# Performance work log

Hardware: AMD Instinct MI355X
Metric: run time of the kernel (lower is better)

Reference implementation:

```python
import jax, jax.numpy as jnp
import numpy as np

BLOCK_LEN = 64  # chunk length l


def setup_inputs() -> dict:
    key = jax.random.key(0)
    k1, k2, k3 = jax.random.split(key, 3)
    b, s, h, p, n = 8, 4096, 16, 64, 64
    X = jax.random.normal(k1, (b, s, h, p), jnp.float32)
    # A must be negative for numerically stable decays (exp(cumsum diffs) <= 1),
    # matching real Mamba2 where A_log parameterizes a negative decay rate.
    A = -0.1 * jnp.abs(jax.random.normal(k2, (b, s, h), jnp.float32))
    B = jax.random.normal(k3, (b, s, h, n), jnp.float32)
    return {"X": X, "A": A, "B": B}


def reference(X, A, B):
    L = BLOCK_LEN
    b, s, h, p = X.shape
    n = B.shape[-1]
    c = s // L  # number of chunks

    # b (c l) ... -> b c l ...
    Xb = X.reshape(b, c, L, h, p)
    Bb = B.reshape(b, c, L, h, n)
    Ab = jnp.transpose(A.reshape(b, c, L, h), (0, 3, 1, 2))  # (b, h, c, l)

    A_cumsum = jnp.cumsum(Ab, axis=-1)  # (b, h, c, l)

    # Fused decay-einsum: states[b,c,h,p,n] =
    #   sum_l B[b,c,l,h,n] * exp(A_cumsum[b,h,c,-1] - A_cumsum[b,h,c,l]) * X[b,c,l,h,p]
    decay_states = jnp.exp(A_cumsum[..., -1:] - A_cumsum)  # (b, h, c, l)
    states = jnp.einsum('bclhn,bhcl,bclhp->bchpn', Bb, decay_states, Xb)

    # Prepend zero initial states along chunk dim -> (b, c+1, h, p, n)
    states = jnp.concatenate([jnp.zeros_like(states[:, :1]), states], axis=1)

    # Inter-chunk recurrence via exp(segsum(padded chunk totals)).
    padded_A = jnp.pad(A_cumsum[..., -1], ((0, 0), (0, 0), (1, 0)))  # (b, h, c+1)
    cs = jnp.cumsum(padded_A, axis=-1)
    Z = c + 1
    diff = cs[..., :, None] - cs[..., None, :]  # (b, h, Z, Z), row - col
    mask = jnp.tril(jnp.ones((Z, Z), dtype=bool))  # row >= col
    decay_chunk = jnp.where(mask, jnp.exp(diff), 0.0)  # (b, h, Z, Z)

    new_states = jnp.einsum('bhzc,bchpn->bzhpn', decay_chunk, states)
    return new_states[:, -1]  # (b, h, p, n)
```

## Files before the change

kernel.cpp:

```cpp
#include <hip/hip_runtime.h>
#include <hip/hip_bf16.h>


constexpr int Bn = 8;
constexpr int S  = 4096;
constexpr int H  = 16;
constexpr int P  = 64;
constexpr int N  = 64;

constexpr int NCH = 8;
constexpr int TCH = S / NCH;
constexpr int TB  = 8;

__global__ __launch_bounds__(256) void scan_weights(
    const float* __restrict__ A, float* __restrict__ W) {
  const int pair = blockIdx.x;
  const int bb = pair / H, hh = pair % H;
  const int tid = threadIdx.x;
  constexpr int TPT = S / 256;

  float vals[TPT];
  float local = 0.f;
  const int t0 = tid * TPT;
  #pragma unroll
  for (int i = 0; i < TPT; ++i) {
    float a = A[((size_t)bb * S + t0 + i) * H + hh];
    local += a;
    vals[i] = local;
  }

  __shared__ float sums[256];
  sums[tid] = local;
  __syncthreads();
  for (int off = 1; off < 256; off <<= 1) {
    float v = sums[tid];
    float add = (tid >= off) ? sums[tid - off] : 0.f;
    __syncthreads();
    sums[tid] = v + add;
    __syncthreads();
  }
  const float total = sums[255];
  const float excl  = sums[tid] - local;

  float* Wp = W + (size_t)pair * S;
  #pragma unroll
  for (int i = 0; i < TPT; ++i) {
    Wp[t0 + i] = __expf(total - (excl + vals[i]));
  }
}

__global__ __launch_bounds__(256) void outer_accum(
    const float* __restrict__ X, const float* __restrict__ Bm,
    const float* __restrict__ W, float* __restrict__ out) {
  __shared__ float Xs[TB][P];
  __shared__ float Bs[TB][N];

  const int bid  = blockIdx.x;
  const int pair = bid / NCH;
  const int ch   = bid % NCH;
  const int tid  = threadIdx.x;
  const int t_begin = ch * TCH;

  const int n0 = (tid & 15) * 4;
  const int p0 = (tid >> 4) * 4;

  const int lrow = (tid & 127) >> 4;
  const int lcol = (tid & 15) * 4;
  const bool isB = tid >= 128;

  const int bb = pair / H, hh = pair % H;
  const size_t baseX = ((size_t)bb * S * H + hh) * (size_t)P;
  const size_t baseB = ((size_t)bb * S * H + hh) * (size_t)N;
  const float* Wp = W + (size_t)pair * S;

  float acc[4][4];
  #pragma unroll
  for (int i = 0; i < 4; ++i)
    #pragma unroll
    for (int j = 0; j < 4; ++j) acc[i][j] = 0.f;

  for (int t0 = t_begin; t0 < t_begin + TCH; t0 += TB) {
    const int t = t0 + lrow;
    if (!isB) {
      const float w = Wp[t];
      const float4 v = *(const float4*)(X + baseX + (size_t)t * H * P + lcol);
      float4 sv; sv.x = v.x * w; sv.y = v.y * w; sv.z = v.z * w; sv.w = v.w * w;
      *(float4*)&Xs[lrow][lcol] = sv;
    } else {
      *(float4*)&Bs[lrow][lcol] = *(const float4*)(Bm + baseB + (size_t)t * H * N + lcol);
    }
    __syncthreads();

    #pragma unroll
    for (int tt = 0; tt < TB; ++tt) {
      const float4 xv = *(const float4*)&Xs[tt][p0];
      const float4 bv = *(const float4*)&Bs[tt][n0];
      const float xs[4] = {xv.x, xv.y, xv.z, xv.w};
      const float bs[4] = {bv.x, bv.y, bv.z, bv.w};
      #pragma unroll
      for (int i = 0; i < 4; ++i)
        #pragma unroll
        for (int j = 0; j < 4; ++j)
          acc[i][j] = fmaf(xs[i], bs[j], acc[i][j]);
    }
    __syncthreads();
  }

  float* outp = out + (size_t)pair * P * N;
  #pragma unroll
  for (int i = 0; i < 4; ++i)
    #pragma unroll
    for (int j = 0; j < 4; ++j)
      atomicAdd(&outp[(size_t)(p0 + i) * N + (n0 + j)], acc[i][j]);
}

extern "C" void kernel_launch(void* const* d_in, const int* in_sizes, int n_in,
                              void* d_out, int out_size, void* d_ws, size_t ws_size,
                              hipStream_t stream) {
  const float* X = (const float*)d_in[0];
  const float* A = (const float*)d_in[1];
  const float* B = (const float*)d_in[2];
  float* out = (float*)d_out;
  float* W   = (float*)d_ws;

  hipMemsetAsync(d_out, 0, (size_t)out_size * sizeof(float), stream);

  scan_weights<<<Bn * H, 256, 0, stream>>>(A, W);
  outer_accum<<<Bn * H * NCH, 256, 0, stream>>>(X, B, W, out);
}
```

Baseline: 327.4 us.

## Double-buffer outer-product accumulation with 8x8 register tiles and per-wave time split

```diff
diff --git a/kernel.cpp b/kernel.cpp
--- a/kernel.cpp
+++ b/kernel.cpp
@@ -1,5 +1,4 @@
 #include <hip/hip_runtime.h>
-#include <hip/hip_bf16.h>
 
 
 constexpr int Bn = 8;
@@ -10,7 +9,8 @@
 
 constexpr int NCH = 8;
 constexpr int TCH = S / NCH;
-constexpr int TB  = 8;
+constexpr int TB  = 32;
+constexpr int NIT = TCH / TB;
 
 __global__ __launch_bounds__(256) void scan_weights(
     const float* __restrict__ A, float* __restrict__ W) {
@@ -49,69 +49,138 @@
   }
 }
 
-__global__ __launch_bounds__(256) void outer_accum(
+__global__ __launch_bounds__(256, 4) void outer_accum(
     const float* __restrict__ X, const float* __restrict__ Bm,
     const float* __restrict__ W, float* __restrict__ out) {
-  __shared__ float Xs[TB][P];
-  __shared__ float Bs[TB][N];
+  __shared__ float4 lds[2][1024];
 
   const int bid  = blockIdx.x;
   const int pair = bid / NCH;
   const int ch   = bid % NCH;
   const int tid  = threadIdx.x;
+  const int lane = tid & 63;
+  const int wid  = tid >> 6;
   const int t_begin = ch * TCH;
 
-  const int n0 = (tid & 15) * 4;
-  const int p0 = (tid >> 4) * 4;
+  const int pr = (lane >> 3) * 8;
+  const int nc = (lane & 7) * 8;
 
-  const int lrow = (tid & 127) >> 4;
-  const int lcol = (tid & 15) * 4;
-  const bool isB = tid >= 128;
+  const int srow = tid >> 4;
+  const int scol = (tid & 15) * 4;
 
   const int bb = pair / H, hh = pair % H;
-  const size_t baseX = ((size_t)bb * S * H + hh) * (size_t)P;
-  const size_t baseB = ((size_t)bb * S * H + hh) * (size_t)N;
+  const float* Xp = X  + (size_t)bb * S * H * P + (size_t)hh * P + scol;
+  const float* Bp = Bm + (size_t)bb * S * H * N + (size_t)hh * N + scol;
   const float* Wp = W + (size_t)pair * S;
 
-  float acc[4][4];
+  float4 rx0, rx1, rb0, rb1;
+  float w0, w1;
+
+  auto LOAD = [&](int t0) {
+    const int ta = t0 + srow;
+    const int tb = ta + 16;
+    w0 = Wp[ta];
+    w1 = Wp[tb];
+    rx0 = *(const float4*)(Xp + (size_t)ta * (H * P));
+    rx1 = *(const float4*)(Xp + (size_t)tb * (H * P));
+    rb0 = *(const float4*)(Bp + (size_t)ta * (H * N));
+    rb1 = *(const float4*)(Bp + (size_t)tb * (H * N));
+  };
+  auto STORE = [&](int buf) {
+    float4 a = rx0; a.x *= w0; a.y *= w0; a.z *= w0; a.w *= w0;
+    float4 b = rx1; b.x *= w1; b.y *= w1; b.z *= w1; b.w *= w1;
+    lds[buf][tid]       = a;
+    lds[buf][256 + tid] = b;
+    lds[buf][512 + tid] = rb0;
+    lds[buf][768 + tid] = rb1;
+  };
+
+  float acc[8][8];
   #pragma unroll
-  for (int i = 0; i < 4; ++i)
+  for (int i = 0; i < 8; ++i)
     #pragma unroll
-    for (int j = 0; j < 4; ++j) acc[i][j] = 0.f;
+    for (int k = 0; k < 8; ++k) acc[i][k] = 0.f;
 
-  for (int t0 = t_begin; t0 < t_begin + TCH; t0 += TB) {
-    const int t = t0 + lrow;
-    if (!isB) {
-      const float w = Wp[t];
-      const float4 v = *(const float4*)(X + baseX + (size_t)t * H * P + lcol);
-      float4 sv; sv.x = v.x * w; sv.y = v.y * w; sv.z = v.z * w; sv.w = v.w * w;
-      *(float4*)&Xs[lrow][lcol] = sv;
-    } else {
-      *(float4*)&Bs[lrow][lcol] = *(const float4*)(Bm + baseB + (size_t)t * H * N + lcol);
+  LOAD(t_begin);
+  STORE(0);
+  __syncthreads();
+
+  for (int it = 0; it < NIT; ++it) {
+    const int cur = it & 1;
+    if (it + 1 < NIT) LOAD(t_begin + (it + 1) * TB);
+
+    const float* Xs = (const float*)&lds[cur][0];
+    const float* Bs = (const float*)&lds[cur][512];
+    #pragma unroll
+    for (int j = 0; j < 8; ++j) {
+      const int tt = (j << 2) | wid;
+      const float4 xa = *(const float4*)(Xs + tt * 64 + pr);
+      const float4 xb = *(const float4*)(Xs + tt * 64 + pr + 4);
+      const float4 ba = *(const float4*)(Bs + tt * 64 + nc);
+      const float4 bc = *(const float4*)(Bs + tt * 64 + nc + 4);
+      const float xs[8] = {xa.x, xa.y, xa.z, xa.w, xb.x, xb.y, xb.z, xb.w};
+      const float bs[8] = {ba.x, ba.y, ba.z, ba.w, bc.x, bc.y, bc.z, bc.w};
+      #pragma unroll
+      for (int i = 0; i < 8; ++i)
+        #pragma unroll
+        for (int k = 0; k < 8; ++k)
+          acc[i][k] = fmaf(xs[i], bs[k], acc[i][k]);
     }
-    __syncthreads();
 
-    #pragma unroll
-    for (int tt = 0; tt < TB; ++tt) {
-      const float4 xv = *(const float4*)&Xs[tt][p0];
-      const float4 bv = *(const float4*)&Bs[tt][n0];
-      const float xs[4] = {xv.x, xv.y, xv.z, xv.w};
-      const float bs[4] = {bv.x, bv.y, bv.z, bv.w};
-      #pragma unroll
-      for (int i = 0; i < 4; ++i)
-        #pragma unroll
-        for (int j = 0; j < 4; ++j)
-          acc[i][j] = fmaf(xs[i], bs[j], acc[i][j]);
+    if (it + 1 < NIT) {
+      STORE((it + 1) & 1);
+      __syncthreads();
     }
-    __syncthreads();
   }
 
-  float* outp = out + (size_t)pair * P * N;
-  #pragma unroll
-  for (int i = 0; i < 4; ++i)
+  __syncthreads();
+  float4* red = (float4*)&lds[0][0];
+
+  if (wid & 1) {
+    float4* r = red + ((wid >> 1) ? 1024 : 0) + lane;
     #pragma unroll
-    for (int j = 0; j < 4; ++j)
-      atomicAdd(&outp[(size_t)(p0 + i) * N + (n0 + j)], acc[i][j]);
+    for (int i = 0; i < 8; ++i) {
+      r[(2 * i + 0) * 64] = make_float4(acc[i][0], acc[i][1], acc[i][2], acc[i][3]);
+      r[(2 * i + 1) * 64] = make_float4(acc[i][4], acc[i][5], acc[i][6], acc[i][7]);
+    }
+  }
+  __syncthreads();
+  if (!(wid & 1)) {
+    const float4* r = red + ((wid >> 1) ? 1024 : 0) + lane;
+    #pragma unroll
+    for (int i = 0; i < 8; ++i) {
+      const float4 v0 = r[(2 * i + 0) * 64];
+      const float4 v1 = r[(2 * i + 1) * 64];
+      acc[i][0] += v0.x; acc[i][1] += v0.y; acc[i][2] += v0.z; acc[i][3] += v0.w;
+      acc[i][4] += v1.x; acc[i][5] += v1.y; acc[i][6] += v1.z; acc[i][7] += v1.w;
+    }
+  }
+  __syncthreads();
+  if (wid == 2) {
+    float4* r = red + lane;
+    #pragma unroll
+    for (int i = 0; i < 8; ++i) {
+      r[(2 * i + 0) * 64] = make_float4(acc[i][0], acc[i][1], acc[i][2], acc[i][3]);
+      r[(2 * i + 1) * 64] = make_float4(acc[i][4], acc[i][5], acc[i][6], acc[i][7]);
+    }
+  }
+  __syncthreads();
+  if (wid == 0) {
+    const float4* r = red + lane;
+    #pragma unroll
+    for (int i = 0; i < 8; ++i) {
+      const float4 v0 = r[(2 * i + 0) * 64];
+      const float4 v1 = r[(2 * i + 1) * 64];
+      acc[i][0] += v0.x; acc[i][1] += v0.y; acc[i][2] += v0.z; acc[i][3] += v0.w;
+      acc[i][4] += v1.x; acc[i][5] += v1.y; acc[i][6] += v1.z; acc[i][7] += v1.w;
+    }
+    float* outp = out + (size_t)pair * P * N;
+    #pragma unroll
+    for (int i = 0; i < 8; ++i)
+      #pragma unroll
+      for (int k = 0; k < 8; ++k)
+        atomicAdd(&outp[(size_t)(pr + i) * N + (nc + k)], acc[i][k]);
+  }
 }
 
 extern "C" void kernel_launch(void* const* d_in, const int* in_sizes, int n_in,
```

Result: slower. 394.1 us (+20.4%).

## Use split-bf16 MFMA (3-pass hi/lo) for chunk outer-product accumulation

Applied to the files above, without the earlier changes.

```diff
diff --git a/kernel.cpp b/kernel.cpp
--- a/kernel.cpp
+++ b/kernel.cpp
@@ -1,5 +1,4 @@
 #include <hip/hip_runtime.h>
-#include <hip/hip_bf16.h>
 
 
 constexpr int Bn = 8;
@@ -10,7 +9,11 @@
 
 constexpr int NCH = 8;
 constexpr int TCH = S / NCH;
-constexpr int TB  = 8;
+constexpr int TB  = 32;
+constexpr int NIT = TCH / TB;
+
+typedef __attribute__((ext_vector_type(4))) float f32x4;
+typedef __attribute__((ext_vector_type(8))) short short8;
 
 __global__ __launch_bounds__(256) void scan_weights(
     const float* __restrict__ A, float* __restrict__ W) {
@@ -49,69 +52,136 @@
   }
 }
 
+__device__ __forceinline__ unsigned pack_hilo(float x) {
+  unsigned bx = __float_as_uint(x);
+  unsigned hi = bx >> 16;
+  float rf = x - __uint_as_float(bx & 0xFFFF0000u);
+  unsigned lo = __float_as_uint(rf) & 0xFFFF0000u;
+  return hi | lo;
+}
+
+__device__ __forceinline__ short8 mk_frag(unsigned a0, unsigned a1,
+                                          unsigned a2, unsigned a3) {
+  union { unsigned u[4]; short8 s; } u;
+  u.u[0] = a0; u.u[1] = a1; u.u[2] = a2; u.u[3] = a3;
+  return u.s;
+}
+
 __global__ __launch_bounds__(256) void outer_accum(
     const float* __restrict__ X, const float* __restrict__ Bm,
     const float* __restrict__ W, float* __restrict__ out) {
-  __shared__ float Xs[TB][P];
-  __shared__ float Bs[TB][N];
+  __shared__ unsigned Xl[64 * 33];
+  __shared__ unsigned Bl[64 * 33];
 
   const int bid  = blockIdx.x;
   const int pair = bid / NCH;
   const int ch   = bid % NCH;
   const int tid  = threadIdx.x;
+  const int lane = tid & 63;
+  const int wid  = __builtin_amdgcn_readfirstlane(tid >> 6);
   const int t_begin = ch * TCH;
 
-  const int n0 = (tid & 15) * 4;
-  const int p0 = (tid >> 4) * 4;
-
-  const int lrow = (tid & 127) >> 4;
-  const int lcol = (tid & 15) * 4;
-  const bool isB = tid >= 128;
-
   const int bb = pair / H, hh = pair % H;
-  const size_t baseX = ((size_t)bb * S * H + hh) * (size_t)P;
-  const size_t baseB = ((size_t)bb * S * H + hh) * (size_t)N;
-  const float* Wp = W + (size_t)pair * S;
-
-  float acc[4][4];
-  #pragma unroll
-  for (int i = 0; i < 4; ++i)
-    #pragma unroll
-    for (int j = 0; j < 4; ++j) acc[i][j] = 0.f;
-
-  for (int t0 = t_begin; t0 < t_begin + TCH; t0 += TB) {
-    const int t = t0 + lrow;
-    if (!isB) {
-      const float w = Wp[t];
-      const float4 v = *(const float4*)(X + baseX + (size_t)t * H * P + lcol);
-      float4 sv; sv.x = v.x * w; sv.y = v.y * w; sv.z = v.z * w; sv.w = v.w * w;
-      *(float4*)&Xs[lrow][lcol] = sv;
-    } else {
-      *(float4*)&Bs[lrow][lcol] = *(const float4*)(Bm + baseB + (size_t)t * H * N + lcol);
-    }
-    __syncthreads();
-
-    #pragma unroll
-    for (int tt = 0; tt < TB; ++tt) {
-      const float4 xv = *(const float4*)&Xs[tt][p0];
-      const float4 bv = *(const float4*)&Bs[tt][n0];
-      const float xs[4] = {xv.x, xv.y, xv.z, xv.w};
-      const float bs[4] = {bv.x, bv.y, bv.z, bv.w};
-      #pragma unroll
-      for (int i = 0; i < 4; ++i)
-        #pragma unroll
-        for (int j = 0; j < 4; ++j)
-          acc[i][j] = fmaf(xs[i], bs[j], acc[i][j]);
-    }
+  constexpr int HP = H * P;
+  constexpr int HN = H * N;
+
+  const float* gXc = X  + (size_t)bb * S * HP + (size_t)hh * P + lane;
+  const float* gBc = Bm + (size_t)bb * S * HN + (size_t)hh * N + lane;
+  const float* Wp  = W + (size_t)pair * S;
+
+  const int m0 = (wid & 1) * 32;
+  const int n0 = (wid >> 1) * 32;
+  const int l15 = lane & 15;
+  const int l4  = lane >> 4;
+
+  f32x4 acc[2][2];
+  #pragma unroll
+  for (int mt = 0; mt < 2; ++mt)
+    #pragma unroll
+    for (int nt = 0; nt < 2; ++nt) acc[mt][nt] = (f32x4)0.f;
+
+  for (int it = 0; it < NIT; ++it) {
+    const int tb = t_begin + it * TB;
+    const int tw = tb + wid * 8;
+
+    float xr[8], br[8], wv[8];
+    #pragma unroll
+    for (int k = 0; k < 8; ++k) {
+      xr[k] = gXc[(size_t)(tw + k) * HP];
+      br[k] = gBc[(size_t)(tw + k) * HN];
+      wv[k] = Wp[tw + k];
+    }
+
+    const int trow = wid * 8;
+    #pragma unroll
+    for (int k = 0; k < 8; ++k) {
+      Xl[lane * 33 + trow + k] = pack_hilo(xr[k] * wv[k]);
+      Bl[lane * 33 + trow + k] = pack_hilo(br[k]);
+    }
+    __syncthreads();
+
+    unsigned ca[2][8], cb[2][8];
+    #pragma unroll
+    for (int mt = 0; mt < 2; ++mt) {
+      const int base = (m0 + mt * 16 + l15) * 33 + l4 * 8;
+      #pragma unroll
+      for (int j = 0; j < 8; ++j) ca[mt][j] = Xl[base + j];
+    }
+    #pragma unroll
+    for (int nt = 0; nt < 2; ++nt) {
+      const int base = (n0 + nt * 16 + l15) * 33 + l4 * 8;
+      #pragma unroll
+      for (int j = 0; j < 8; ++j) cb[nt][j] = Bl[base + j];
+    }
+
+    short8 ahi[2], alo[2], bhi[2], blo[2];
+    #pragma unroll
+    for (int mt = 0; mt < 2; ++mt) {
+      ahi[mt] = mk_frag(__builtin_amdgcn_perm(ca[mt][1], ca[mt][0], 0x05040100),
+                        __builtin_amdgcn_perm(ca[mt][3], ca[mt][2], 0x05040100),
+                        __builtin_amdgcn_perm(ca[mt][5], ca[mt][4], 0x05040100),
+                        __builtin_amdgcn_perm(ca[mt][7], ca[mt][6], 0x05040100));
+      alo[mt] = mk_frag(__builtin_amdgcn_perm(ca[mt][1], ca[mt][0], 0x07060302),
+                        __builtin_amdgcn_perm(ca[mt][3], ca[mt][2], 0x07060302),
+                        __builtin_amdgcn_perm(ca[mt][5], ca[mt][4], 0x07060302),
+                        __builtin_amdgcn_perm(ca[mt][7], ca[mt][6], 0x07060302));
+    }
+    #pragma unroll
+    for (int nt = 0; nt < 2; ++nt) {
+      bhi[nt] = mk_frag(__builtin_amdgcn_perm(cb[nt][1], cb[nt][0], 0x05040100),
+                        __builtin_amdgcn_perm(cb[nt][3], cb[nt][2], 0x05040100),
+                        __builtin_amdgcn_perm(cb[nt][5], cb[nt][4], 0x05040100),
+                        __builtin_amdgcn_perm(cb[nt][7], cb[nt][6], 0x05040100));
+      blo[nt] = mk_frag(__builtin_amdgcn_perm(cb[nt][1], cb[nt][0], 0x07060302),
+                        __builtin_amdgcn_perm(cb[nt][3], cb[nt][2], 0x07060302),
+                        __builtin_amdgcn_perm(cb[nt][5], cb[nt][4], 0x07060302),
+                        __builtin_amdgcn_perm(cb[nt][7], cb[nt][6], 0x07060302));
+    }
+
+    #pragma unroll
+    for (int mt = 0; mt < 2; ++mt)
+      #pragma unroll
+      for (int nt = 0; nt < 2; ++nt) {
+        f32x4 c = acc[mt][nt];
+        c = __builtin_amdgcn_mfma_f32_16x16x32_bf16(alo[mt], bhi[nt], c, 0, 0, 0);
+        c = __builtin_amdgcn_mfma_f32_16x16x32_bf16(ahi[mt], blo[nt], c, 0, 0, 0);
+        c = __builtin_amdgcn_mfma_f32_16x16x32_bf16(ahi[mt], bhi[nt], c, 0, 0, 0);
+        acc[mt][nt] = c;
+      }
     __syncthreads();
   }
 
   float* outp = out + (size_t)pair * P * N;
   #pragma unroll
-  for (int i = 0; i < 4; ++i)
-    #pragma unroll
-    for (int j = 0; j < 4; ++j)
-      atomicAdd(&outp[(size_t)(p0 + i) * N + (n0 + j)], acc[i][j]);
+  for (int mt = 0; mt < 2; ++mt)
+    #pragma unroll
+    for (int nt = 0; nt < 2; ++nt) {
+      const int p = m0 + mt * 16 + l4 * 4;
+      const int n = n0 + nt * 16 + l15;
+      #pragma unroll
+      for (int r = 0; r < 4; ++r)
+        atomicAdd(&outp[(size_t)(p + r) * N + n], acc[mt][nt][r]);
+    }
 }
 
 extern "C" void kernel_launch(void* const* d_in, const int* in_sizes, int n_in,
```

Result: faster. 296.1 us (-9.6%).
